# Kernel tuning notes

Hardware: AMD Instinct MI355X
Metric: run time of the kernel (lower is better)

The kernel has to match this reference:

```python
import jax, jax.numpy as jnp
import numpy as np

HEADS = 16
HEAD_DIM = 64
EMBED = HEADS * HEAD_DIM  # 1024
N, L = 4, 4096


def setup_inputs() -> dict:
    key = jax.random.key(0)
    k1, k2, k3, k4, k5, k6, k7, k8 = jax.random.split(key, 8)
    s = 0.02
    return {
        "q": jax.random.normal(k1, (N, L, EMBED), jnp.float32),
        "k": jax.random.normal(k2, (N, L, EMBED), jnp.float32),
        "v": jax.random.normal(k3, (N, L, EMBED), jnp.float32),
        "mask": jnp.ones((N, L, HEADS, HEADS), jnp.int32),
        # torch Linear weights: (out_features, in_features)
        "q_w": jax.random.normal(k4, (HEAD_DIM, HEAD_DIM), jnp.float32) * s,
        "k_w": jax.random.normal(k5, (HEAD_DIM, HEAD_DIM), jnp.float32) * s,
        "v_w": jax.random.normal(k6, (HEAD_DIM, HEAD_DIM), jnp.float32) * s,
        "fc_w": jax.random.normal(k7, (EMBED, EMBED), jnp.float32) * s,
        "fc_b": jax.random.normal(k8, (EMBED,), jnp.float32) * s,
    }


def reference(q, k, v, mask, q_w, k_w, v_w, fc_w, fc_b):
    n, ql = q.shape[0], q.shape[1]
    # reshape to (N, L, H, D) and apply per-head-dim linear projections (x @ W.T)
    q4 = q.reshape(n, ql, HEADS, HEAD_DIM) @ q_w.T
    k4 = k.reshape(n, k.shape[1], HEADS, HEAD_DIM) @ k_w.T
    v4 = v.reshape(n, v.shape[1], HEADS, HEAD_DIM) @ v_w.T
    # Faithful to the original: matmul broadcasts over (N, L), contracting head_dim,
    # so logits are (N, L, H, H) -- attention across heads per token.
    scale = 1.0 / jnp.sqrt(jnp.float32(HEAD_DIM))
    logits = jnp.einsum("nlhd,nlgd->nlhg", q4, k4) * scale
    logits = jnp.where(mask == 0, -jnp.inf, logits)
    weights = jax.nn.softmax(logits, axis=-1)
    out4 = jnp.einsum("nlhg,nlgd->nlhd", weights, v4)  # (N, L, H, D)
    # Faithful scrambled reshape: permute to (N, H, L, D) then flatten to (N, L, H*D)
    out = out4.transpose(0, 2, 1, 3).reshape(n, ql, HEADS * HEAD_DIM)
    return out @ fc_w.T + fc_b
```

## Files before the change

kernel.cpp:

```cpp
#include <hip/hip_runtime.h>
#include <hip/hip_bf16.h>
#include <stdint.h>

#define TOKENS 16384
#define LSEQ 4096
#define WPAD 72

typedef short bf16x8 __attribute__((ext_vector_type(8)));
typedef float f32x4 __attribute__((ext_vector_type(4)));

typedef __attribute__((address_space(1))) void as1_t;
typedef __attribute__((address_space(3))) void as3_t;

__device__ __forceinline__ unsigned short f2bf(float x) {
  __hip_bfloat16 t = __float2bfloat16(x);
  return *reinterpret_cast<unsigned short*>(&t);
}

__device__ __forceinline__ bf16x8 pack8(float4 a, float4 b) {
  bf16x8 t;
  t[0] = (short)f2bf(a.x); t[1] = (short)f2bf(a.y);
  t[2] = (short)f2bf(a.z); t[3] = (short)f2bf(a.w);
  t[4] = (short)f2bf(b.x); t[5] = (short)f2bf(b.y);
  t[6] = (short)f2bf(b.z); t[7] = (short)f2bf(b.w);
  return t;
}

__device__ __forceinline__ void async16(const void* g, void* lds) {
  __builtin_amdgcn_global_load_lds((as1_t*)const_cast<void*>(g),
                                   (as3_t*)lds, 16, 0, 0);
}
#define WAITCNT(n) asm volatile("s_waitcnt vmcnt(" #n ")" ::: "memory")

__global__ __launch_bounds__(256) void cvt_prep(
    const float* __restrict__ fcw, unsigned short* __restrict__ Wb,
    const float* __restrict__ qw, const float* __restrict__ kw,
    const float* __restrict__ vw, unsigned short* __restrict__ Mout,
    unsigned short* __restrict__ vwout) {
  const int b = blockIdx.x, t = threadIdx.x;
  if (b < 1024) {
    const int i = b * 256 + t;
    float4 f = ((const float4*)fcw)[i];
    union { unsigned short us[4]; uint2 u2; } pk;
    pk.us[0] = f2bf(f.x); pk.us[1] = f2bf(f.y);
    pk.us[2] = f2bf(f.z); pk.us[3] = f2bf(f.w);
    ((uint2*)Wb)[i] = pk.u2;
    return;
  }
  __shared__ float ql[4096], kl[4096];
#pragma unroll
  for (int j = 0; j < 4; ++j) {
    const int i = t + j * 256;
    ((float4*)ql)[i] = ((const float4*)qw)[i];
    ((float4*)kl)[i] = ((const float4*)kw)[i];
    float4 f = ((const float4*)vw)[i];
    union { unsigned short us[4]; uint2 u2; } pk;
    pk.us[0] = f2bf(f.x); pk.us[1] = f2bf(f.y);
    pk.us[2] = f2bf(f.z); pk.us[3] = f2bf(f.w);
    ((uint2*)vwout)[i] = pk.u2;
  }
  __syncthreads();
  const int f = t >> 2;
  const int e0 = (t & 3) * 16;
  float4 a0 = {}, a1 = {}, a2 = {}, a3 = {};
#pragma unroll 8
  for (int d = 0; d < 64; ++d) {
    const float qv = ql[d * 64 + f];
    const float* kr = &kl[d * 64 + e0];
    const float4 k0 = *(const float4*)(kr);
    const float4 k1 = *(const float4*)(kr + 4);
    const float4 k2 = *(const float4*)(kr + 8);
    const float4 k3 = *(const float4*)(kr + 12);
    a0.x += qv * k0.x; a0.y += qv * k0.y; a0.z += qv * k0.z; a0.w += qv * k0.w;
    a1.x += qv * k1.x; a1.y += qv * k1.y; a1.z += qv * k1.z; a1.w += qv * k1.w;
    a2.x += qv * k2.x; a2.y += qv * k2.y; a2.z += qv * k2.z; a2.w += qv * k2.w;
    a3.x += qv * k3.x; a3.y += qv * k3.y; a3.z += qv * k3.z; a3.w += qv * k3.w;
  }
  union { unsigned short us[8]; uint4 u4; } p0, p1;
  p0.us[0] = f2bf(a0.x); p0.us[1] = f2bf(a0.y); p0.us[2] = f2bf(a0.z); p0.us[3] = f2bf(a0.w);
  p0.us[4] = f2bf(a1.x); p0.us[5] = f2bf(a1.y); p0.us[6] = f2bf(a1.z); p0.us[7] = f2bf(a1.w);
  p1.us[0] = f2bf(a2.x); p1.us[1] = f2bf(a2.y); p1.us[2] = f2bf(a2.z); p1.us[3] = f2bf(a2.w);
  p1.us[4] = f2bf(a3.x); p1.us[5] = f2bf(a3.y); p1.us[6] = f2bf(a3.z); p1.us[7] = f2bf(a3.w);
  *(uint4*)&Mout[f * 64 + e0] = p0.u4;
  *(uint4*)&Mout[f * 64 + e0 + 8] = p1.u4;
}

__global__ __launch_bounds__(256, 6) void attn11(
    const float* __restrict__ q, const float* __restrict__ k,
    const float* __restrict__ v, const int* __restrict__ mask,
    const unsigned short* __restrict__ Mg, const unsigned short* __restrict__ vwg,
    unsigned short* __restrict__ X) {
  __shared__ unsigned short Ml[64 * WPAD];
  __shared__ unsigned short Vw[64 * WPAD];
  __shared__ unsigned short scr[4][16 * WPAD];

  const int tid = threadIdx.x;
  const int l = tid & 63, w = tid >> 6;
  const int lr = l & 15, lg = l >> 4;

  const int tok = blockIdx.x * 4 + w;
  const size_t tb = (size_t)tok * 1024;
  const int off = lr * 64 + lg * 8;

  const float4 qa = *(const float4*)(q + tb + off);
  const float4 qb = *(const float4*)(q + tb + off + 4);
  const float4 qc = *(const float4*)(q + tb + off + 32);
  const float4 qd = *(const float4*)(q + tb + off + 36);
  const float4 ka = *(const float4*)(k + tb + off);
  const float4 kb = *(const float4*)(k + tb + off + 4);
  const float4 kc = *(const float4*)(k + tb + off + 32);
  const float4 kd = *(const float4*)(k + tb + off + 36);
  const float4 va = *(const float4*)(v + tb + off);
  const float4 vb = *(const float4*)(v + tb + off + 4);
  const float4 vc = *(const float4*)(v + tb + off + 32);
  const float4 vd = *(const float4*)(v + tb + off + 36);
  const int4 mk4 = *(const int4*)(mask + (size_t)tok * 256 + lr * 16 + lg * 4);

  {
    const int row = tid >> 2, c0 = (tid & 3) * 16;
    *(uint4*)&Ml[row * WPAD + c0]     = *(const uint4*)(Mg + row * 64 + c0);
    *(uint4*)&Ml[row * WPAD + c0 + 8] = *(const uint4*)(Mg + row * 64 + c0 + 8);
    *(uint4*)&Vw[row * WPAD + c0]     = *(const uint4*)(vwg + row * 64 + c0);
    *(uint4*)&Vw[row * WPAD + c0 + 8] = *(const uint4*)(vwg + row * 64 + c0 + 8);
  }
  __syncthreads();

  const bf16x8 ak0 = pack8(ka, kb), ak1 = pack8(kc, kd);
  const bf16x8 av0 = pack8(va, vb), av1 = pack8(vc, vd);
  const bf16x8 aq0 = pack8(qa, qb), aq1 = pack8(qc, qd);

  f32x4 accu[4], accv[4];
#pragma unroll
  for (int n = 0; n < 4; ++n) {
    const int wrow = (n * 16 + lr) * WPAD;
    f32x4 z = {};
    const bf16x8 bm0 = *(const bf16x8*)&Ml[wrow + lg * 8];
    const bf16x8 bm1 = *(const bf16x8*)&Ml[wrow + 32 + lg * 8];
    accu[n] = __builtin_amdgcn_mfma_f32_16x16x32_bf16(ak0, bm0, z, 0, 0, 0);
    accu[n] = __builtin_amdgcn_mfma_f32_16x16x32_bf16(ak1, bm1, accu[n], 0, 0, 0);
    const bf16x8 bw0 = *(const bf16x8*)&Vw[wrow + lg * 8];
    const bf16x8 bw1 = *(const bf16x8*)&Vw[wrow + 32 + lg * 8];
    accv[n] = __builtin_amdgcn_mfma_f32_16x16x32_bf16(av0, bw0, z, 0, 0, 0);
    accv[n] = __builtin_amdgcn_mfma_f32_16x16x32_bf16(av1, bw1, accv[n], 0, 0, 0);
  }

  unsigned short* U = scr[w];
#pragma unroll
  for (int n = 0; n < 4; ++n)
#pragma unroll
    for (int r = 0; r < 4; ++r)
      U[(lg * 4 + r) * WPAD + n * 16 + lr] = f2bf(accu[n][r]);

  const bf16x8 ua0 = *(const bf16x8*)&U[lr * WPAD + lg * 8];
  const bf16x8 ua1 = *(const bf16x8*)&U[lr * WPAD + 32 + lg * 8];
  f32x4 z4 = {};
  f32x4 st = __builtin_amdgcn_mfma_f32_16x16x32_bf16(ua0, aq0, z4, 0, 0, 0);
  st = __builtin_amdgcn_mfma_f32_16x16x32_bf16(ua1, aq1, st, 0, 0, 0);

  float e[4];
  float sm = 0.f;
  const int mks[4] = {mk4.x, mk4.y, mk4.z, mk4.w};
#pragma unroll
  for (int r = 0; r < 4; ++r) {
    e[r] = (mks[r] != 0) ? __expf(st[r] * 0.125f) : 0.f;
    sm += e[r];
  }
  sm += __shfl_xor(sm, 16);
  sm += __shfl_xor(sm, 32);
  const float inv = 1.0f / sm;
#pragma unroll
  for (int r = 0; r < 4; ++r) e[r] *= inv;

  bf16x8 apv;
#pragma unroll
  for (int j = 0; j < 8; ++j) {
    const int srcg = (lg * 2 + (j >> 2)) & 3;
    const float pv = __shfl(e[j & 3], lr + srcg * 16, 64);
    apv[j] = (short)((lg < 2) ? f2bf(pv) : (unsigned short)0);
  }

  const int s0 = lr + ((lg & 1) * 2) * 16;
  const int s1 = s0 + 16;
  f32x4 o[4];
#pragma unroll
  for (int n = 0; n < 4; ++n) {
    bf16x8 bv;
#pragma unroll
    for (int j = 0; j < 8; ++j) {
      const float xv = __shfl(accv[n][j & 3], (j < 4) ? s0 : s1, 64);
      bv[j] = (short)f2bf(xv);
    }
    f32x4 z = {};
    o[n] = __builtin_amdgcn_mfma_f32_16x16x32_bf16(apv, bv, z, 0, 0, 0);
  }

#pragma unroll
  for (int n = 0; n < 4; ++n)
#pragma unroll
    for (int r = 0; r < 4; ++r)
      U[(lg * 4 + r) * WPAD + n * 16 + lr] = f2bf(o[n][r]);

  const int nb = tok >> 12, lpos = tok & (LSEQ - 1);
#pragma unroll
  for (int it = 0; it < 2; ++it) {
    const int idx = it * 64 + l;
    const int h = idx >> 3, c = idx & 7;
    const uint4 val = *(const uint4*)&U[h * WPAD + c * 8];
    *(uint4*)&X[((size_t)(nb * 16 + h) * LSEQ + lpos) * 64 + c * 8] = val;
  }
}

__global__ __launch_bounds__(512, 1) void gemm_fc8(
    const unsigned short* __restrict__ A,
    const unsigned short* __restrict__ B,
    const float* __restrict__ bias,
    float* __restrict__ C) {
  __shared__ char lds[131072];

  const int tid = threadIdx.x;
  const int l = tid & 63;
  const int wv = tid >> 6;
  const int wr = wv >> 2;
  const int wc = wv & 3;
  const int lr = l & 15, lg = l >> 4;

  const int bid = blockIdx.x;
  const int wg = (bid & 7) * 32 + (bid >> 3);
  const int tm = (wg >> 2) * 256;
  const int tn = (wg & 3) * 256;

  const int srow = wv * 8 + (l >> 3);
  const int schunk = (l & 7) ^ (2 * ((l >> 5) & 1));

  auto stage_unit = [&](int u) {
    const int kt = u >> 2, t = u & 3, h = t & 1;
    const unsigned short* src =
        (t < 2) ? (A + (size_t)(tm + h * 128) * 1024)
                : (B + (size_t)(tn + h * 128) * 1024);
    const int k0 = kt * 64;
    char* dst = lds + (u & 7) * 16384 + wv * 1024;
#pragma unroll
    for (int li = 0; li < 2; ++li) {
      const int r = li * 64 + srow;
      async16(src + (size_t)r * 1024 + k0 + schunk * 8, dst + li * 8192);
    }
  };

#pragma unroll
  for (int u = 0; u < 4; ++u) stage_unit(u);
  WAITCNT(0);
  __builtin_amdgcn_s_barrier();

  f32x4 acc[8][4] = {};
  const int swz = ((lr >> 2) & 1) * 32;
  const int arow0 = lr * 128;
  const int brow0 = ((wc & 1) * 64 + lr) * 128;

#pragma unroll 1
  for (int j = 0; j < 16; ++j) {
    const char* abase = lds + ((j & 1) * 4 + wr) * 16384;
    const char* bbase = lds + ((j & 1) * 4 + 2 + (wc >> 1)) * 16384;
    bf16x8 bfr[4], af[4];

#pragma unroll
    for (int fj = 0; fj < 4; ++fj)
      bfr[fj] = *(const bf16x8*)(bbase + brow0 + fj * 2048 + ((lg * 16) ^ swz));
#pragma unroll
    for (int mi = 0; mi < 4; ++mi)
      af[mi] = *(const bf16x8*)(abase + arow0 + mi * 2048 + ((lg * 16) ^ swz));
    if (j < 15) stage_unit(4 * j + 4);
    __builtin_amdgcn_sched_barrier(0);
    __builtin_amdgcn_s_barrier();
    __builtin_amdgcn_s_setprio(1);
#pragma unroll
    for (int mi = 0; mi < 4; ++mi)
#pragma unroll
      for (int fj = 0; fj < 4; ++fj)
        acc[mi][fj] = __builtin_amdgcn_mfma_f32_16x16x32_bf16(af[mi], bfr[fj],
                                                              acc[mi][fj], 0, 0, 0);
    __builtin_amdgcn_s_setprio(0);
    __builtin_amdgcn_s_barrier();

#pragma unroll
    for (int mi = 0; mi < 4; ++mi)
      af[mi] = *(const bf16x8*)(abase + arow0 + 8192 + mi * 2048 + ((lg * 16) ^ swz));
    if (j < 15) stage_unit(4 * j + 5);
    __builtin_amdgcn_sched_barrier(0);
    __builtin_amdgcn_s_barrier();
    __builtin_amdgcn_s_setprio(1);
#pragma unroll
    for (int mi = 0; mi < 4; ++mi)
#pragma unroll
      for (int fj = 0; fj < 4; ++fj)
        acc[4 + mi][fj] = __builtin_amdgcn_mfma_f32_16x16x32_bf16(af[mi], bfr[fj],
                                                                  acc[4 + mi][fj], 0, 0, 0);
    __builtin_amdgcn_s_setprio(0);
    __builtin_amdgcn_s_barrier();

#pragma unroll
    for (int fj = 0; fj < 4; ++fj)
      bfr[fj] = *(const bf16x8*)(bbase + brow0 + fj * 2048 + ((64 + lg * 16) ^ swz));
#pragma unroll
    for (int mi = 0; mi < 4; ++mi)
      af[mi] = *(const bf16x8*)(abase + arow0 + mi * 2048 + ((64 + lg * 16) ^ swz));
    if (j < 15) stage_unit(4 * j + 6);
    __builtin_amdgcn_sched_barrier(0);
    __builtin_amdgcn_s_barrier();
    __builtin_amdgcn_s_setprio(1);
#pragma unroll
    for (int mi = 0; mi < 4; ++mi)
#pragma unroll
      for (int fj = 0; fj < 4; ++fj)
        acc[mi][fj] = __builtin_amdgcn_mfma_f32_16x16x32_bf16(af[mi], bfr[fj],
                                                              acc[mi][fj], 0, 0, 0);
    __builtin_amdgcn_s_setprio(0);
    __builtin_amdgcn_s_barrier();

#pragma unroll
    for (int mi = 0; mi < 4; ++mi)
      af[mi] = *(const bf16x8*)(abase + arow0 + 8192 + mi * 2048 + ((64 + lg * 16) ^ swz));
    if (j < 15) stage_unit(4 * j + 7);
    __builtin_amdgcn_sched_barrier(0);
    __builtin_amdgcn_s_barrier();
    __builtin_amdgcn_s_setprio(1);
#pragma unroll
    for (int mi = 0; mi < 4; ++mi)
#pragma unroll
      for (int fj = 0; fj < 4; ++fj)
        acc[4 + mi][fj] = __builtin_amdgcn_mfma_f32_16x16x32_bf16(af[mi], bfr[fj],
                                                                  acc[4 + mi][fj], 0, 0, 0);
    __builtin_amdgcn_s_setprio(0);
    if (j < 15) {
      WAITCNT(0);
      __builtin_amdgcn_s_barrier();
    }
  }

#pragma unroll
  for (int fj = 0; fj < 4; ++fj) {
    const int col = tn + wc * 64 + fj * 16 + lr;
    const float bv = bias[col];
#pragma unroll
    for (int mf = 0; mf < 8; ++mf)
#pragma unroll
      for (int rr = 0; rr < 4; ++rr) {
        const int row = tm + wr * 128 + mf * 16 + lg * 4 + rr;
        C[(size_t)row * 1024 + col] = acc[mf][fj][rr] + bv;
      }
  }
}

extern "C" void kernel_launch(void* const* d_in, const int* in_sizes, int n_in,
                              void* d_out, int out_size, void* d_ws, size_t ws_size,
                              hipStream_t stream) {
  (void)in_sizes; (void)n_in; (void)out_size; (void)ws_size;
  const float* q   = (const float*)d_in[0];
  const float* k   = (const float*)d_in[1];
  const float* v   = (const float*)d_in[2];
  const int*  mask = (const int*)d_in[3];
  const float* qw  = (const float*)d_in[4];
  const float* kw  = (const float*)d_in[5];
  const float* vw  = (const float*)d_in[6];
  const float* fcw = (const float*)d_in[7];
  const float* fcb = (const float*)d_in[8];
  float* out = (float*)d_out;

  unsigned short* X   = (unsigned short*)d_ws;
  unsigned short* Wb  = X + (size_t)16 * 1024 * 1024;
  unsigned short* Mw  = Wb + (size_t)1024 * 1024;
  unsigned short* vwb = Mw + 4096;

  cvt_prep<<<dim3(1025), dim3(256), 0, stream>>>(fcw, Wb, qw, kw, vw, Mw, vwb);
  attn11<<<dim3(4096), dim3(256), 0, stream>>>(q, k, v, mask, Mw, vwb, X);
  gemm_fc8<<<dim3(256), dim3(512), 0, stream>>>(X, Wb, fcb, out);
}
```

Before: 102.3 us.

## Fold fc weight conversion into attention kernel and enlarge attention blocks to 16 tokens

The fc weight bf16 conversion moves out of the prep kernel into extra blocks of the attention kernel, so the prep kernel becomes a single small block that computes only the q/k fused matrix and the v weights. The attention kernel now runs 1024-thread blocks covering 16 tokens each, which amortizes the per-block load of the small weight matrices into LDS across more tokens. The intent is to take fc conversion off the critical path and reduce redundant weight staging. In exchange, the larger blocks use more LDS and drop the previous occupancy hint, which may lower how many waves can be resident per CU.

Measured after the change: 105.9 us. +3.5%, slower.

```diff
diff --git a/kernel.cpp b/kernel.cpp
--- a/kernel.cpp
+++ b/kernel.cpp
@@ -32,14 +32,52 @@
 }
 #define WAITCNT(n) asm volatile("s_waitcnt vmcnt(" #n ")" ::: "memory")
 
-__global__ __launch_bounds__(256) void cvt_prep(
-    const float* __restrict__ fcw, unsigned short* __restrict__ Wb,
+__global__ __launch_bounds__(1024) void prep_weights(
     const float* __restrict__ qw, const float* __restrict__ kw,
     const float* __restrict__ vw, unsigned short* __restrict__ Mout,
     unsigned short* __restrict__ vwout) {
-  const int b = blockIdx.x, t = threadIdx.x;
-  if (b < 1024) {
-    const int i = b * 256 + t;
+  __shared__ float ql[4096], kl[4096];
+  const int t = threadIdx.x;
+  ((float4*)ql)[t] = ((const float4*)qw)[t];
+  ((float4*)kl)[t] = ((const float4*)kw)[t];
+  {
+    float4 f = ((const float4*)vw)[t];
+    union { unsigned short us[4]; uint2 u2; } pk;
+    pk.us[0] = f2bf(f.x); pk.us[1] = f2bf(f.y);
+    pk.us[2] = f2bf(f.z); pk.us[3] = f2bf(f.w);
+    ((uint2*)vwout)[t] = pk.u2;
+  }
+  __syncthreads();
+  const int f = t >> 4;
+  const int e0 = (t & 15) * 4;
+  float acc0 = 0.f, acc1 = 0.f, acc2 = 0.f, acc3 = 0.f;
+#pragma unroll 8
+  for (int d = 0; d < 64; ++d) {
+    const float qv = ql[d * 64 + f];
+    const float4 kv = *(const float4*)&kl[d * 64 + e0];
+    acc0 += qv * kv.x; acc1 += qv * kv.y; acc2 += qv * kv.z; acc3 += qv * kv.w;
+  }
+  union { unsigned short us[4]; uint2 u2; } pk;
+  pk.us[0] = f2bf(acc0); pk.us[1] = f2bf(acc1);
+  pk.us[2] = f2bf(acc2); pk.us[3] = f2bf(acc3);
+  *(uint2*)&Mout[f * 64 + e0] = pk.u2;
+}
+
+__global__ __launch_bounds__(1024) void attn_cvt(
+    const float* __restrict__ q, const float* __restrict__ k,
+    const float* __restrict__ v, const int* __restrict__ mask,
+    const unsigned short* __restrict__ Mg, const unsigned short* __restrict__ vwg,
+    unsigned short* __restrict__ X,
+    const float* __restrict__ fcw, unsigned short* __restrict__ Wb) {
+  __shared__ unsigned short Ml[64 * WPAD];
+  __shared__ unsigned short Vw[64 * WPAD];
+  __shared__ unsigned short scr[16][16 * WPAD];
+
+  const int b = blockIdx.x;
+  const int tid = threadIdx.x;
+
+  if (b >= 1024) {
+    const int i = (b - 1024) * 1024 + tid;
     float4 f = ((const float4*)fcw)[i];
     union { unsigned short us[4]; uint2 u2; } pk;
     pk.us[0] = f2bf(f.x); pk.us[1] = f2bf(f.y);
@@ -47,58 +85,11 @@
     ((uint2*)Wb)[i] = pk.u2;
     return;
   }
-  __shared__ float ql[4096], kl[4096];
-#pragma unroll
-  for (int j = 0; j < 4; ++j) {
-    const int i = t + j * 256;
-    ((float4*)ql)[i] = ((const float4*)qw)[i];
-    ((float4*)kl)[i] = ((const float4*)kw)[i];
-    float4 f = ((const float4*)vw)[i];
-    union { unsigned short us[4]; uint2 u2; } pk;
-    pk.us[0] = f2bf(f.x); pk.us[1] = f2bf(f.y);
-    pk.us[2] = f2bf(f.z); pk.us[3] = f2bf(f.w);
-    ((uint2*)vwout)[i] = pk.u2;
-  }
-  __syncthreads();
-  const int f = t >> 2;
-  const int e0 = (t & 3) * 16;
-  float4 a0 = {}, a1 = {}, a2 = {}, a3 = {};
-#pragma unroll 8
-  for (int d = 0; d < 64; ++d) {
-    const float qv = ql[d * 64 + f];
-    const float* kr = &kl[d * 64 + e0];
-    const float4 k0 = *(const float4*)(kr);
-    const float4 k1 = *(const float4*)(kr + 4);
-    const float4 k2 = *(const float4*)(kr + 8);
-    const float4 k3 = *(const float4*)(kr + 12);
-    a0.x += qv * k0.x; a0.y += qv * k0.y; a0.z += qv * k0.z; a0.w += qv * k0.w;
-    a1.x += qv * k1.x; a1.y += qv * k1.y; a1.z += qv * k1.z; a1.w += qv * k1.w;
-    a2.x += qv * k2.x; a2.y += qv * k2.y; a2.z += qv * k2.z; a2.w += qv * k2.w;
-    a3.x += qv * k3.x; a3.y += qv * k3.y; a3.z += qv * k3.z; a3.w += qv * k3.w;
-  }
-  union { unsigned short us[8]; uint4 u4; } p0, p1;
-  p0.us[0] = f2bf(a0.x); p0.us[1] = f2bf(a0.y); p0.us[2] = f2bf(a0.z); p0.us[3] = f2bf(a0.w);
-  p0.us[4] = f2bf(a1.x); p0.us[5] = f2bf(a1.y); p0.us[6] = f2bf(a1.z); p0.us[7] = f2bf(a1.w);
-  p1.us[0] = f2bf(a2.x); p1.us[1] = f2bf(a2.y); p1.us[2] = f2bf(a2.z); p1.us[3] = f2bf(a2.w);
-  p1.us[4] = f2bf(a3.x); p1.us[5] = f2bf(a3.y); p1.us[6] = f2bf(a3.z); p1.us[7] = f2bf(a3.w);
-  *(uint4*)&Mout[f * 64 + e0] = p0.u4;
-  *(uint4*)&Mout[f * 64 + e0 + 8] = p1.u4;
-}
-
-__global__ __launch_bounds__(256, 6) void attn11(
-    const float* __restrict__ q, const float* __restrict__ k,
-    const float* __restrict__ v, const int* __restrict__ mask,
-    const unsigned short* __restrict__ Mg, const unsigned short* __restrict__ vwg,
-    unsigned short* __restrict__ X) {
-  __shared__ unsigned short Ml[64 * WPAD];
-  __shared__ unsigned short Vw[64 * WPAD];
-  __shared__ unsigned short scr[4][16 * WPAD];
-
-  const int tid = threadIdx.x;
+
   const int l = tid & 63, w = tid >> 6;
   const int lr = l & 15, lg = l >> 4;
 
-  const int tok = blockIdx.x * 4 + w;
+  const int tok = b * 16 + w;
   const size_t tb = (size_t)tok * 1024;
   const int off = lr * 64 + lg * 8;
 
@@ -117,11 +108,11 @@
   const int4 mk4 = *(const int4*)(mask + (size_t)tok * 256 + lr * 16 + lg * 4);
 
   {
-    const int row = tid >> 2, c0 = (tid & 3) * 16;
-    *(uint4*)&Ml[row * WPAD + c0]     = *(const uint4*)(Mg + row * 64 + c0);
-    *(uint4*)&Ml[row * WPAD + c0 + 8] = *(const uint4*)(Mg + row * 64 + c0 + 8);
-    *(uint4*)&Vw[row * WPAD + c0]     = *(const uint4*)(vwg + row * 64 + c0);
-    *(uint4*)&Vw[row * WPAD + c0 + 8] = *(const uint4*)(vwg + row * 64 + c0 + 8);
+    const int row = (tid & 511) >> 3, c0 = (tid & 7) * 8;
+    if (tid < 512)
+      *(uint4*)&Ml[row * WPAD + c0] = *(const uint4*)(Mg + row * 64 + c0);
+    else
+      *(uint4*)&Vw[row * WPAD + c0] = *(const uint4*)(vwg + row * 64 + c0);
   }
   __syncthreads();
 
@@ -370,7 +361,7 @@
   unsigned short* Mw  = Wb + (size_t)1024 * 1024;
   unsigned short* vwb = Mw + 4096;
 
-  cvt_prep<<<dim3(1025), dim3(256), 0, stream>>>(fcw, Wb, qw, kw, vw, Mw, vwb);
-  attn11<<<dim3(4096), dim3(256), 0, stream>>>(q, k, v, mask, Mw, vwb, X);
+  prep_weights<<<dim3(1), dim3(1024), 0, stream>>>(qw, kw, vw, Mw, vwb);
+  attn_cvt<<<dim3(1280), dim3(1024), 0, stream>>>(q, k, v, mask, Mw, vwb, X, fcw, Wb);
   gemm_fc8<<<dim3(256), dim3(512), 0, stream>>>(X, Wb, fcb, out);
 }
```
